# Kernel optimization log

Hardware: AMD Instinct MI355X
Metric: run time of the kernel (lower is better)

Reference implementation:

```python
import jax, jax.numpy as jnp
import numpy as np

GAMMA = 1.0
N, M, D = 1024, 128, 128  # M must equal embed_dim D for the original numpy broadcast


def setup_inputs() -> dict:
    key = jax.random.key(0)
    k1, k2, k3, k4 = jax.random.split(key, 4)
    a = jax.random.normal(k1, (N, D), dtype=jnp.float32)
    b = jax.random.normal(k2, (M, D), dtype=jnp.float32)
    rotation_params = jax.random.normal(k3, (D, D), dtype=jnp.float32)
    entangle_params = jax.random.normal(k4, (D, D), dtype=jnp.float32)
    return {"a": a, "b": b, "rotation_params": rotation_params,
            "entangle_params": entangle_params}


def reference(a, b, rotation_params, entangle_params):
    d = a.shape[-1]
    # --- RBF Gram matrix (replaces nested python loops): ||x-y||^2 expansion ---
    sq = (jnp.sum(a * a, axis=1)[:, None]
          + jnp.sum(b * b, axis=1)[None, :]
          - 2.0 * (a @ b.T))                      # [N, M]
    K = jnp.exp(-GAMMA * sq)                       # [N, M]
    # --- batched self-attention, each row of `a` is a length-1 sequence ---
    q = a @ rotation_params.reshape(d, -1)         # [N, d]
    k = a @ entangle_params.reshape(d, -1)         # [N, d]
    logits = jnp.sum(q * k, axis=-1, keepdims=True) / float(np.sqrt(d))  # [N, 1]
    scores = jax.nn.softmax(logits, axis=-1)       # == 1 (single key per query)
    attn_weights = scores * a                      # [N, d] (scores @ value for len-1 seq)
    # --- K * attn_weights[:, None]: numpy broadcast (N,M)*(N,1,d) -> (N,N,d) ---
    # out[i, j, kk] = K[j, kk] * attn_weights[i, kk]
    return K[None, :, :] * attn_weights[:, None, :]  # [N, N, D]
```

## Files before the change

kernel.cpp:

```cpp
#include <hip/hip_runtime.h>
#include <math.h>


#define GAMMA_F 1.0f
#define N_ROWS 1024
#define DIM    128

__global__ __launch_bounds__(DIM) void compute_K_kernel(
    const float* __restrict__ a,
    const float* __restrict__ b,
    float* __restrict__ K)
{
    __shared__ float4 a_sh[DIM / 4];
    const int j = blockIdx.x;
    const int m = threadIdx.x;

    if (m < DIM / 4) {
        a_sh[m] = reinterpret_cast<const float4*>(a + (size_t)j * DIM)[m];
    }
    __syncthreads();

    const float4* b4 = reinterpret_cast<const float4*>(b + (size_t)m * DIM);
    float acc = 0.0f;
#pragma unroll 8
    for (int d = 0; d < DIM / 4; ++d) {
        const float4 av = a_sh[d];
        const float4 bv = b4[d];
        const float dx = av.x - bv.x;
        const float dy = av.y - bv.y;
        const float dz = av.z - bv.z;
        const float dw = av.w - bv.w;
        acc = fmaf(dx, dx, acc);
        acc = fmaf(dy, dy, acc);
        acc = fmaf(dz, dz, acc);
        acc = fmaf(dw, dw, acc);
    }
    K[(size_t)j * DIM + m] = expf(-GAMMA_F * acc);
}

__global__ __launch_bounds__(256) void bcast_mul_kernel(
    const float4* __restrict__ a4,
    const float4* __restrict__ K4,
    float4* __restrict__ out4,
    unsigned n_vec)
{
    const unsigned v = blockIdx.x * 256u + threadIdx.x;
    if (v >= n_vec) return;

    const unsigned k4  = v & 31u;
    const unsigned row = v >> 5;
    const unsigned j   = row & 1023u;
    const unsigned i   = row >> 10;

    const float4 av = a4[i * 32u + k4];
    const float4 kv = K4[j * 32u + k4];

    float4 o;
    o.x = av.x * kv.x;
    o.y = av.y * kv.y;
    o.z = av.z * kv.z;
    o.w = av.w * kv.w;
    out4[v] = o;
}

extern "C" void kernel_launch(void* const* d_in, const int* in_sizes, int n_in,
                              void* d_out, int out_size, void* d_ws, size_t ws_size,
                              hipStream_t stream)
{
    const float* a = reinterpret_cast<const float*>(d_in[0]);
    const float* b = reinterpret_cast<const float*>(d_in[1]);

    float* K = reinterpret_cast<float*>(d_ws);

    compute_K_kernel<<<N_ROWS, DIM, 0, stream>>>(a, b, K);

    const unsigned n_vec = (unsigned)(out_size / 4);
    const unsigned blocks = (n_vec + 255u) / 256u;
    bcast_mul_kernel<<<blocks, 256, 0, stream>>>(
        reinterpret_cast<const float4*>(a),
        reinterpret_cast<const float4*>(K),
        reinterpret_cast<float4*>(d_out),
        n_vec);
}
```

Baseline: 537.5 us.

## Coarsen broadcast-multiply per thread and use nontemporal stores for output

The broadcast multiply kernel now assigns each block one row i and a 128-row slice of K. Each thread loads its row of a once and writes 16 output vectors using nontemporal stores, so the 512 MB output stream bypasses cache pollution. The grid drops from one thread per output vector to 8192 blocks, which cuts index arithmetic and repeated loads of a. In exchange there is less parallelism per element and the code now hardcodes the problem sizes.

```diff
diff --git a/kernel.cpp b/kernel.cpp
--- a/kernel.cpp
+++ b/kernel.cpp
@@ -6,26 +6,28 @@
 #define N_ROWS 1024
 #define DIM    128
 
+typedef float f32x4 __attribute__((ext_vector_type(4)));
+
 __global__ __launch_bounds__(DIM) void compute_K_kernel(
     const float* __restrict__ a,
     const float* __restrict__ b,
     float* __restrict__ K)
 {
-    __shared__ float4 a_sh[DIM / 4];
+    __shared__ f32x4 a_sh[DIM / 4];
     const int j = blockIdx.x;
     const int m = threadIdx.x;
 
     if (m < DIM / 4) {
-        a_sh[m] = reinterpret_cast<const float4*>(a + (size_t)j * DIM)[m];
+        a_sh[m] = reinterpret_cast<const f32x4*>(a + (size_t)j * DIM)[m];
     }
     __syncthreads();
 
-    const float4* b4 = reinterpret_cast<const float4*>(b + (size_t)m * DIM);
+    const f32x4* b4 = reinterpret_cast<const f32x4*>(b + (size_t)m * DIM);
     float acc = 0.0f;
 #pragma unroll 8
     for (int d = 0; d < DIM / 4; ++d) {
-        const float4 av = a_sh[d];
-        const float4 bv = b4[d];
+        const f32x4 av = a_sh[d];
+        const f32x4 bv = b4[d];
         const float dx = av.x - bv.x;
         const float dy = av.y - bv.y;
         const float dz = av.z - bv.z;
@@ -39,28 +41,26 @@
 }
 
 __global__ __launch_bounds__(256) void bcast_mul_kernel(
-    const float4* __restrict__ a4,
-    const float4* __restrict__ K4,
-    float4* __restrict__ out4,
-    unsigned n_vec)
+    const f32x4* __restrict__ a4,
+    const f32x4* __restrict__ K4,
+    f32x4* __restrict__ out4)
 {
-    const unsigned v = blockIdx.x * 256u + threadIdx.x;
-    if (v >= n_vec) return;
+    const int i   = blockIdx.x >> 3;
+    const int j0  = (blockIdx.x & 7) << 7;
+    const int k4  = threadIdx.x & 31;
+    const int sub = threadIdx.x >> 5;
 
-    const unsigned k4  = v & 31u;
-    const unsigned row = v >> 5;
-    const unsigned j   = row & 1023u;
-    const unsigned i   = row >> 10;
+    const f32x4 av = a4[i * 32 + k4];
 
-    const float4 av = a4[i * 32u + k4];
-    const float4 kv = K4[j * 32u + k4];
+    const f32x4* __restrict__ Kp = K4 + (size_t)(j0 + sub) * 32 + k4;
+    f32x4* __restrict__ Op = out4 + ((size_t)i * 1024 + j0 + sub) * 32 + k4;
 
-    float4 o;
-    o.x = av.x * kv.x;
-    o.y = av.y * kv.y;
-    o.z = av.z * kv.z;
-    o.w = av.w * kv.w;
-    out4[v] = o;
+#pragma unroll
+    for (int jj = 0; jj < 16; ++jj) {
+        const f32x4 kv = Kp[(size_t)jj * 8 * 32];
+        f32x4 o = av * kv;
+        __builtin_nontemporal_store(o, &Op[(size_t)jj * 8 * 32]);
+    }
 }
 
 extern "C" void kernel_launch(void* const* d_in, const int* in_sizes, int n_in,
@@ -74,11 +74,8 @@
 
     compute_K_kernel<<<N_ROWS, DIM, 0, stream>>>(a, b, K);
 
-    const unsigned n_vec = (unsigned)(out_size / 4);
-    const unsigned blocks = (n_vec + 255u) / 256u;
-    bcast_mul_kernel<<<blocks, 256, 0, stream>>>(
-        reinterpret_cast<const float4*>(a),
-        reinterpret_cast<const float4*>(K),
-        reinterpret_cast<float4*>(d_out),
-        n_vec);
+    bcast_mul_kernel<<<N_ROWS * 8, 256, 0, stream>>>(
+        reinterpret_cast<const f32x4*>(a),
+        reinterpret_cast<const f32x4*>(K),
+        reinterpret_cast<f32x4*>(d_out));
 }
```

Measured after the change: 540.0 us. Within noise of the previous version (+0.5%).
